# Performance work log

Measured on AMD Instinct MI355X. Metric: run time of the kernel, lower is better.

Reference implementation:

```python
import jax, jax.numpy as jnp
import numpy as np

N = 50000          # nodes
E = 1600000        # edges
H = 8              # heads
F = 16             # out feats per head (np1class)
IN = 256           # in feats
NEG_SLOPE = 0.2    # DGL GATConv default leaky_relu slope


def setup_inputs() -> dict:
    key = jax.random.key(0)
    ks = jax.random.split(key, 7)
    x = jax.random.normal(ks[0], (N, IN), dtype=jnp.float32)
    W = jax.random.normal(ks[1], (IN, H * F), dtype=jnp.float32) * 0.05
    attn_l = jax.random.normal(ks[2], (H, F), dtype=jnp.float32) * 0.05
    attn_r = jax.random.normal(ks[3], (H, F), dtype=jnp.float32) * 0.05
    bias = jax.random.normal(ks[4], (H * F,), dtype=jnp.float32) * 0.05
    src = jax.random.randint(ks[5], (E,), 0, N, dtype=jnp.int64)
    dst = jax.random.randint(ks[6], (E,), 0, N, dtype=jnp.int64)
    return {"x": x, "W": W, "attn_l": attn_l, "attn_r": attn_r,
            "bias": bias, "src": src, "dst": dst}


def reference(x, W, attn_l, attn_r, bias, src, dst):
    # Linear projection to heads: [N, H, F]
    feat = (x @ W).reshape(N, H, F)
    # Per-node attention halves: [N, H]
    el = jnp.einsum('nhf,hf->nh', feat, attn_l)
    er = jnp.einsum('nhf,hf->nh', feat, attn_r)
    # Edge scores: e = leaky_relu(el[src] + er[dst])  -> [E, H]
    e = jax.nn.leaky_relu(el[src] + er[dst], negative_slope=NEG_SLOPE)
    # Segment softmax over incoming edges of each destination node
    m = jax.ops.segment_max(e, dst, num_segments=N)           # [N, H]
    m = jnp.where(jnp.isfinite(m), m, 0.0)                    # empty segments
    m = jax.lax.stop_gradient(m)
    ex = jnp.exp(e - m[dst])                                  # [E, H]
    s = jax.ops.segment_sum(ex, dst, num_segments=N)          # [N, H]
    a = ex / jnp.maximum(s[dst], 1e-9)                        # [E, H]
    # Weighted aggregation of source features: [N, H, F]
    msg = a[:, :, None] * feat[src]
    rst = jax.ops.segment_sum(msg, dst, num_segments=N)
    rst = rst + bias.reshape(H, F)
    # Classifier: mean over heads -> [N, F]
    return rst.mean(axis=1)
```

## Files before the change

### kernel.cpp

```cpp
#include <hip/hip_runtime.h>
#include <hip/hip_bf16.h>

#define NH 8
#define NF 16
#define NIN 256
#define HF 128
#define CAP 3072
#define BCH 4096

typedef __attribute__((ext_vector_type(8))) short bf16x8;
typedef __attribute__((ext_vector_type(4))) float f32x4;

__device__ __forceinline__ unsigned short f2bf(float f) {
    union { float f; unsigned int u; } v; v.f = f;
    unsigned int r = v.u + 0x7FFFu + ((v.u >> 16) & 1u);
    return (unsigned short)(r >> 16);
}
__device__ __forceinline__ float bf2f(unsigned short b) {
    union { unsigned int u; float f; } v; v.u = ((unsigned int)b) << 16;
    return v.f;
}

struct GemmLds {
    union {
        struct {
            unsigned short AsH[32][264];
            unsigned short AsL[32][264];
        };
        float scratch[32][132];
    };
};
struct CsrLds {
    unsigned int eary[CAP];
    unsigned short sSrc[CAP];
    unsigned short roff[512];
    unsigned short rcntl[512];
    int rbase[512];
    int len[64], cur[64];
    unsigned int wsum[4];
    unsigned int sbase;
};
#define POOLSZ ((sizeof(GemmLds) > sizeof(CsrLds)) ? sizeof(GemmLds) : sizeof(CsrLds))

#define GROWS 128
__device__ __forceinline__ void gemm_body(char* pool, int bid,
                                          const float* __restrict__ A,
                                          const float* __restrict__ W,
                                          const float* __restrict__ attn_l,
                                          const float* __restrict__ attn_r,
                                          unsigned short* __restrict__ featb,
                                          float* __restrict__ el,
                                          float* __restrict__ er, int M) {
    GemmLds& gl = *reinterpret_cast<GemmLds*>(pool);
    const int tid = threadIdx.x;
    const int wave = tid >> 6, lane = tid & 63;
    const int quad = lane >> 4, lq = lane & 15;
    const int row0 = bid * GROWS;

    bf16x8 bfrag[8][2];
#pragma unroll
    for (int h2 = 0; h2 < 2; h2++) {
        const int col = (wave * 2 + h2) * 16 + lq;
#pragma unroll
        for (int kk = 0; kk < 8; kk++) {
            const int kb = kk * 32 + quad * 8;
            bf16x8 f;
#pragma unroll
            for (int j = 0; j < 8; j++)
                f[j] = (short)f2bf(W[(size_t)(kb + j) * HF + col]);
            bfrag[kk][h2] = f;
        }
    }

    const int srow = tid >> 3;
    const int erow = tid >> 3, eh = tid & 7;

    for (int c = 0; c < 4; c++) {
        const int crow0 = row0 + c * 32;
        __syncthreads();
#pragma unroll
        for (int i = 0; i < 8; i++) {
            const int col = ((tid & 7) + i * 8) * 4;
            const int gr = crow0 + srow;
            float4 v = make_float4(0.f, 0.f, 0.f, 0.f);
            if (gr < M) v = *(const float4*)&A[(size_t)gr * NIN + col];
            const unsigned short h0 = f2bf(v.x), h1 = f2bf(v.y),
                                 h2b = f2bf(v.z), h3 = f2bf(v.w);
            *(ushort4*)&gl.AsH[srow][col] = make_ushort4(h0, h1, h2b, h3);
            *(ushort4*)&gl.AsL[srow][col] =
                make_ushort4(f2bf(v.x - bf2f(h0)), f2bf(v.y - bf2f(h1)),
                             f2bf(v.z - bf2f(h2b)), f2bf(v.w - bf2f(h3)));
        }
        __syncthreads();
        f32x4 accs[2][2];
#pragma unroll
        for (int s = 0; s < 2; s++) {
            f32x4 acc0 = {0.f, 0.f, 0.f, 0.f};
            f32x4 acc1 = {0.f, 0.f, 0.f, 0.f};
            const int ar = s * 16 + lq;
#pragma unroll
            for (int kk = 0; kk < 8; kk++) {
                const bf16x8 ah = *(const bf16x8*)&gl.AsH[ar][kk * 32 + quad * 8];
                const bf16x8 al = *(const bf16x8*)&gl.AsL[ar][kk * 32 + quad * 8];
                acc0 = __builtin_amdgcn_mfma_f32_16x16x32_bf16(ah, bfrag[kk][0], acc0, 0, 0, 0);
                acc1 = __builtin_amdgcn_mfma_f32_16x16x32_bf16(ah, bfrag[kk][1], acc1, 0, 0, 0);
                acc0 = __builtin_amdgcn_mfma_f32_16x16x32_bf16(al, bfrag[kk][0], acc0, 0, 0, 0);
                acc1 = __builtin_amdgcn_mfma_f32_16x16x32_bf16(al, bfrag[kk][1], acc1, 0, 0, 0);
            }
            accs[s][0] = acc0;
            accs[s][1] = acc1;
#pragma unroll
            for (int r = 0; r < 4; r++) {
                const int gr = crow0 + s * 16 + quad * 4 + r;
                if (gr < M) {
                    featb[(size_t)gr * HF + (wave * 2 + 0) * 16 + lq] = f2bf(acc0[r]);
                    featb[(size_t)gr * HF + (wave * 2 + 1) * 16 + lq] = f2bf(acc1[r]);
                }
            }
        }
        __syncthreads();
#pragma unroll
        for (int s = 0; s < 2; s++)
#pragma unroll
            for (int r = 0; r < 4; r++) {
                const int srw = s * 16 + quad * 4 + r;
                gl.scratch[srw][(wave * 2 + 0) * 16 + lq] = accs[s][0][r];
                gl.scratch[srw][(wave * 2 + 1) * 16 + lq] = accs[s][1][r];
            }
        __syncthreads();
        {
            const int gr = crow0 + erow;
            if (gr < M) {
                const float* sr = &gl.scratch[erow][eh * 16];
                float sl = 0.f, srr = 0.f;
#pragma unroll
                for (int f = 0; f < 16; f++) {
                    const float v = sr[f];
                    sl = fmaf(v, attn_l[eh * 16 + f], sl);
                    srr = fmaf(v, attn_r[eh * 16 + f], srr);
                }
                el[(size_t)gr * NH + eh] = sl;
                er[(size_t)gr * NH + eh] = srr;
            }
        }
    }
}

__device__ __forceinline__ void csr_body(char* pool, int b,
                                         const unsigned int* __restrict__ binned,
                                         const unsigned int* __restrict__ runtab,
                                         int* __restrict__ nodeinfo,
                                         unsigned short* __restrict__ srcsw,
                                         int N, int NB, int nbb) {
    CsrLds& cl = *reinterpret_cast<CsrLds*>(pool);
    const int t = threadIdx.x;
    const int node0 = b << 6;
    const int lane = t & 63, w = t >> 6;
    if (t == 0) cl.sbase = 0;
    __syncthreads();
    for (int c0 = 0; c0 < nbb; c0 += 256) {
        const int r = c0 + t;
        const unsigned int e = (r < nbb) ? runtab[(size_t)r * NB + b] : 0;
        const unsigned int v = e >> 16;
        unsigned int incl = v;
#pragma unroll
        for (int off = 1; off < 64; off <<= 1) {
            const unsigned int x = __shfl_up(incl, off, 64);
            if (lane >= off) incl += x;
        }
        if (lane == 63) cl.wsum[w] = incl;
        __syncthreads();
        unsigned int wbase = 0;
        for (int k = 0; k < w; k++) wbase += cl.wsum[k];
        const unsigned int tot = cl.wsum[0] + cl.wsum[1] + cl.wsum[2] + cl.wsum[3];
        if (r < nbb) {
            cl.roff[r] = (unsigned short)(e & 0xFFFFu);
            cl.rcntl[r] = (unsigned short)v;
            cl.rbase[r] = (int)(cl.sbase + wbase + incl - v);
        }
        __syncthreads();
        if (t == 0) cl.sbase += tot;
        __syncthreads();
    }
    const int tot = (int)cl.sbase;
    for (int r = t; r < nbb; r += 256) {
        const int off = (int)cl.roff[r];
        const int pb = cl.rbase[r];
        const int rc = (int)cl.rcntl[r];
        const unsigned int* bp = &binned[(size_t)r * BCH + off];
        for (int j = 0; j < rc; j++) cl.eary[pb + j] = bp[j];
    }
    if (t < 64) cl.len[t] = 0;
    __syncthreads();
    for (int i = t; i < tot; i += 256) atomicAdd(&cl.len[cl.eary[i] >> 16], 1);
    __syncthreads();
    if (t < 64) {
        const int v = cl.len[t];
        int incl = v;
#pragma unroll
        for (int off = 1; off < 64; off <<= 1) {
            const int x = __shfl_up(incl, off, 64);
            if (t >= off) incl += x;
        }
        const int excl = incl - v;
        cl.cur[t] = excl;
        if (node0 + t < N) nodeinfo[node0 + t] = excl | (v << 16);
    }
    __syncthreads();
    for (int i = t; i < tot; i += 256) {
        const unsigned int p = cl.eary[i];
        const int pos = atomicAdd(&cl.cur[p >> 16], 1);
        cl.sSrc[pos] = (unsigned short)(p & 0xFFFFu);
    }
    __syncthreads();
    unsigned short* sw = &srcsw[(size_t)b * CAP];
    for (int i = t; i < tot; i += 256) sw[i] = cl.sSrc[i];
}

__global__ __launch_bounds__(256) void gemm_csr(const float* __restrict__ A,
                                                const float* __restrict__ W,
                                                const float* __restrict__ attn_l,
                                                const float* __restrict__ attn_r,
                                                unsigned short* __restrict__ featb,
                                                float* __restrict__ el,
                                                float* __restrict__ er, int M,
                                                const unsigned int* __restrict__ binned,
                                                const unsigned int* __restrict__ runtab,
                                                int* __restrict__ nodeinfo,
                                                unsigned short* __restrict__ srcsw,
                                                int NB, int nbb, int GB) {
    __shared__ __align__(16) char pool[POOLSZ];
    if ((int)blockIdx.x < GB)
        gemm_body(pool, blockIdx.x, A, W, attn_l, attn_r, featb, el, er, M);
    else
        csr_body(pool, blockIdx.x - GB, binned, runtab, nodeinfo, srcsw, M, NB, nbb);
}

__global__ __launch_bounds__(256) void bin_kernel(const int* __restrict__ src,
                                                  const int* __restrict__ dst,
                                                  unsigned int* __restrict__ binned,
                                                  unsigned int* __restrict__ runtab,
                                                  int E, int NB) {
    __shared__ unsigned int hist[784];
    __shared__ unsigned int offs[784];
    __shared__ unsigned short lpos[BCH];
    __shared__ unsigned int obuf[BCH];
    __shared__ int dcache[BCH];
    __shared__ unsigned int wsum[4];
    __shared__ unsigned int sbase;
    const int blk = blockIdx.x, t = threadIdx.x;
    const int base = blk * BCH;
    const int cnt = min(BCH, E - base);
    const int lane = t & 63, w = t >> 6;
    for (int b = t; b < NB; b += 256) hist[b] = 0;
    for (int i = t; i < cnt; i += 256) dcache[i] = dst[base + i];
    if (t == 0) sbase = 0;
    __syncthreads();
    for (int i = t; i < cnt; i += 256)
        lpos[i] = (unsigned short)atomicAdd(&hist[dcache[i] >> 6], 1u);
    __syncthreads();
    for (int c0 = 0; c0 < NB; c0 += 256) {
        const int idx = c0 + t;
        const unsigned int v = (idx < NB) ? hist[idx] : 0;
        unsigned int incl = v;
#pragma unroll
        for (int off = 1; off < 64; off <<= 1) {
            const unsigned int x = __shfl_up(incl, off, 64);
            if (lane >= off) incl += x;
        }
        if (lane == 63) wsum[w] = incl;
        __syncthreads();
        unsigned int wbase = 0;
        for (int k = 0; k < w; k++) wbase += wsum[k];
        const unsigned int tot = wsum[0] + wsum[1] + wsum[2] + wsum[3];
        const unsigned int excl = sbase + wbase + incl - v;
        if (idx < NB) {
            offs[idx] = excl;
            runtab[(size_t)blk * NB + idx] = excl | (v << 16);
        }
        __syncthreads();
        if (t == 0) sbase += tot;
        __syncthreads();
    }
    for (int i = t; i < cnt; i += 256) {
        const int d = dcache[i];
        obuf[offs[d >> 6] + lpos[i]] =
            (unsigned int)src[base + i] | ((unsigned int)(d & 63) << 16);
    }
    __syncthreads();
    for (int i = t; i < cnt; i += 256) binned[(size_t)base + i] = obuf[i];
}

#define WIN 64
__global__ __launch_bounds__(256) void agg_kernel(const int* __restrict__ nodeinfo,
                                                  const unsigned short* __restrict__ srcsw,
                                                  const float* __restrict__ el,
                                                  const float* __restrict__ er,
                                                  const unsigned short* __restrict__ featb,
                                                  const float* __restrict__ bias,
                                                  float* __restrict__ out, int N) {
    __shared__ float lds_sc[4][WIN][8];
    __shared__ int lds_src[4][WIN];
    const int tid = threadIdx.x;
    const int w = tid >> 6, lane = tid & 63;
    const int n = blockIdx.x * 4 + w;
    if (n >= N) return;

    const int info = nodeinfo[n];
    const int begin = (n >> 6) * CAP + (info & 0xFFFF);
    const int end = begin + (info >> 16);
    const int hA = lane & 7, eA = lane >> 3;
    const float er_h = er[(size_t)n * NH + hA];
    const int hB = lane >> 3, fB2 = lane & 7;

    float2 acc = make_float2(0.f, 0.f);
    float psum = 0.f;
    for (int base = begin; base < end; base += WIN) {
        const int cn = min(WIN, end - base);
        __builtin_amdgcn_wave_barrier();
#pragma unroll
        for (int rep = 0; rep < 8; rep++) {
            const int ei = rep * 8 + eA;
            if (ei < cn) {
                const int si = (int)srcsw[base + ei];
                if (hA == 0) lds_src[w][ei] = si;
                float v = el[(size_t)si * NH + hA] + er_h;
                v = v > 0.f ? v : 0.2f * v;
                const float sc = __expf(v);
                lds_sc[w][ei][hA] = sc;
                psum += sc;
            }
        }
        __builtin_amdgcn_wave_barrier();
        for (int b0 = 0; b0 < cn; b0 += 16) {
            unsigned int fv[16];
#pragma unroll
            for (int j = 0; j < 16; j++) {
                const int ej = b0 + j;
                const int sj = lds_src[w][ej];
                fv[j] = (ej < cn)
                            ? *(const unsigned int*)&featb[(size_t)sj * HF + hB * 16 + fB2 * 2]
                            : 0u;
            }
#pragma unroll
            for (int j = 0; j < 16; j++) {
                const int ej = b0 + j;
                const float sc = (ej < cn) ? lds_sc[w][ej][hB] : 0.f;
                acc.x = fmaf(sc, bf2f((unsigned short)(fv[j] & 0xFFFFu)), acc.x);
                acc.y = fmaf(sc, bf2f((unsigned short)(fv[j] >> 16)), acc.y);
            }
        }
    }

    float s = psum;
    s += __shfl_xor(s, 8, 64);
    s += __shfl_xor(s, 16, 64);
    s += __shfl_xor(s, 32, 64);
    const float s_h = __shfl(s, hB, 64);
    const float inv = 1.f / fmaxf(s_h, 1e-9f);
    float2 val;
    val.x = acc.x * inv + bias[hB * 16 + fB2 * 2];
    val.y = acc.y * inv + bias[hB * 16 + fB2 * 2 + 1];
    val.x += __shfl_xor(val.x, 8, 64);
    val.x += __shfl_xor(val.x, 16, 64);
    val.x += __shfl_xor(val.x, 32, 64);
    val.y += __shfl_xor(val.y, 8, 64);
    val.y += __shfl_xor(val.y, 16, 64);
    val.y += __shfl_xor(val.y, 32, 64);
    if (lane < 8) {
        float2 o;
        o.x = val.x * 0.125f;
        o.y = val.y * 0.125f;
        *(float2*)&out[(size_t)n * 16 + lane * 2] = o;
    }
}

extern "C" void kernel_launch(void* const* d_in, const int* in_sizes, int n_in,
                              void* d_out, int out_size, void* d_ws, size_t ws_size,
                              hipStream_t stream) {
    const float* x      = (const float*)d_in[0];
    const float* W      = (const float*)d_in[1];
    const float* attn_l = (const float*)d_in[2];
    const float* attn_r = (const float*)d_in[3];
    const float* bias   = (const float*)d_in[4];
    const int*   src    = (const int*)d_in[5];
    const int*   dst    = (const int*)d_in[6];
    float* out = (float*)d_out;

    const int N = in_sizes[0] / NIN;
    const int E = in_sizes[5];
    const int NB = (N + 63) >> 6;
    const int nbb = (E + BCH - 1) / BCH;
    const int GB = (N + GROWS - 1) / GROWS;

    char* w = (char*)d_ws;
    unsigned short* featb = (unsigned short*)w; w += (size_t)N * HF * 2;
    float* el     = (float*)w; w += (size_t)N * NH * 4;
    float* er     = (float*)w; w += (size_t)N * NH * 4;
    int* nodeinfo = (int*)w;   w += (size_t)N * 4;
    unsigned int* binned = (unsigned int*)w; w += (size_t)nbb * BCH * 4;
    unsigned int* runtab = (unsigned int*)w; w += (size_t)nbb * NB * 4;
    unsigned short* srcsw = (unsigned short*)w;

    bin_kernel<<<nbb, 256, 0, stream>>>(src, dst, binned, runtab, E, NB);
    gemm_csr<<<GB + NB, 256, 0, stream>>>(x, W, attn_l, attn_r, featb, el, er, N,
                                          binned, runtab, nodeinfo, srcsw, NB, nbb, GB);
    agg_kernel<<<(N + 3) / 4, 256, 0, stream>>>(nodeinfo, srcsw, el, er, featb, bias,
                                                out, N);
}
```

Before: 209.5 us.

## Fuse edge binning into GEMM/CSR kernel with atomic grid barrier

Moves the edge-binning pass into the combined GEMM/CSR kernel. Binning blocks run alongside the GEMM blocks, wait on a global atomic counter until all binning is finished, then each builds two CSR buckets. This removes a separate kernel launch and the serial dependency between binning and the GEMM. It also narrows the cached dst values to 16 bits to shrink LDS. The spin barrier needs every binning block to be resident at once, so it could deadlock on smaller devices, and it adds a memset to reset the counter.

```diff
diff --git a/kernel.cpp b/kernel.cpp
--- a/kernel.cpp
+++ b/kernel.cpp
@@ -29,6 +29,15 @@
         };
         float scratch[32][132];
     };
+};
+struct BinLds {
+    unsigned short dcache[BCH];
+    unsigned short lpos[BCH];
+    unsigned int hist[784];
+    unsigned int offs[784];
+    unsigned int obuf[BCH];
+    unsigned int wsum[4];
+    unsigned int sbase;
 };
 struct CsrLds {
     unsigned int eary[CAP];
@@ -40,7 +49,8 @@
     unsigned int wsum[4];
     unsigned int sbase;
 };
-#define POOLSZ ((sizeof(GemmLds) > sizeof(CsrLds)) ? sizeof(GemmLds) : sizeof(CsrLds))
+#define MAX2(a,b) ((a) > (b) ? (a) : (b))
+#define POOLSZ MAX2(sizeof(BinLds), MAX2(sizeof(GemmLds), sizeof(CsrLds)))
 
 #define GROWS 128
 __device__ __forceinline__ void gemm_body(char* pool, int bid,
@@ -146,6 +156,56 @@
     }
 }
 
+__device__ __forceinline__ void bin_body(char* pool, int blk,
+                                         const int* __restrict__ src,
+                                         const int* __restrict__ dst,
+                                         unsigned int* __restrict__ binned,
+                                         unsigned int* __restrict__ runtab,
+                                         int E, int NB) {
+    BinLds& bl = *reinterpret_cast<BinLds*>(pool);
+    const int t = threadIdx.x;
+    const int base = blk * BCH;
+    const int cnt = min(BCH, E - base);
+    const int lane = t & 63, w = t >> 6;
+    for (int b = t; b < NB; b += 256) bl.hist[b] = 0;
+    for (int i = t; i < cnt; i += 256) bl.dcache[i] = (unsigned short)dst[base + i];
+    if (t == 0) bl.sbase = 0;
+    __syncthreads();
+    for (int i = t; i < cnt; i += 256)
+        bl.lpos[i] = (unsigned short)atomicAdd(&bl.hist[bl.dcache[i] >> 6], 1u);
+    __syncthreads();
+    for (int c0 = 0; c0 < NB; c0 += 256) {
+        const int idx = c0 + t;
+        const unsigned int v = (idx < NB) ? bl.hist[idx] : 0;
+        unsigned int incl = v;
+#pragma unroll
+        for (int off = 1; off < 64; off <<= 1) {
+            const unsigned int x = __shfl_up(incl, off, 64);
+            if (lane >= off) incl += x;
+        }
+        if (lane == 63) bl.wsum[w] = incl;
+        __syncthreads();
+        unsigned int wbase = 0;
+        for (int k = 0; k < w; k++) wbase += bl.wsum[k];
+        const unsigned int tot = bl.wsum[0] + bl.wsum[1] + bl.wsum[2] + bl.wsum[3];
+        const unsigned int excl = bl.sbase + wbase + incl - v;
+        if (idx < NB) {
+            bl.offs[idx] = excl;
+            runtab[(size_t)blk * NB + idx] = excl | (v << 16);
+        }
+        __syncthreads();
+        if (t == 0) bl.sbase += tot;
+        __syncthreads();
+    }
+    for (int i = t; i < cnt; i += 256) {
+        const int d = (int)bl.dcache[i];
+        bl.obuf[bl.offs[d >> 6] + bl.lpos[i]] =
+            (unsigned int)src[base + i] | ((unsigned int)(d & 63) << 16);
+    }
+    __syncthreads();
+    for (int i = t; i < cnt; i += 256) binned[(size_t)base + i] = bl.obuf[i];
+}
+
 __device__ __forceinline__ void csr_body(char* pool, int b,
                                          const unsigned int* __restrict__ binned,
                                          const unsigned int* __restrict__ runtab,
@@ -217,78 +277,37 @@
     for (int i = t; i < tot; i += 256) sw[i] = cl.sSrc[i];
 }
 
-__global__ __launch_bounds__(256) void gemm_csr(const float* __restrict__ A,
-                                                const float* __restrict__ W,
-                                                const float* __restrict__ attn_l,
-                                                const float* __restrict__ attn_r,
-                                                unsigned short* __restrict__ featb,
-                                                float* __restrict__ el,
-                                                float* __restrict__ er, int M,
-                                                const unsigned int* __restrict__ binned,
-                                                const unsigned int* __restrict__ runtab,
-                                                int* __restrict__ nodeinfo,
-                                                unsigned short* __restrict__ srcsw,
-                                                int NB, int nbb, int GB) {
+__global__ __launch_bounds__(256, 4) void gemm_bincsr(
+        const float* __restrict__ A, const float* __restrict__ W,
+        const float* __restrict__ attn_l, const float* __restrict__ attn_r,
+        unsigned short* __restrict__ featb, float* __restrict__ el,
+        float* __restrict__ er, int M,
+        const int* __restrict__ src, const int* __restrict__ dst,
+        unsigned int* __restrict__ binned, unsigned int* __restrict__ runtab,
+        int* __restrict__ nodeinfo, unsigned short* __restrict__ srcsw,
+        unsigned int* __restrict__ done, int E, int NB, int nbb, int GB) {
     __shared__ __align__(16) char pool[POOLSZ];
-    if ((int)blockIdx.x < GB)
-        gemm_body(pool, blockIdx.x, A, W, attn_l, attn_r, featb, el, er, M);
-    else
-        csr_body(pool, blockIdx.x - GB, binned, runtab, nodeinfo, srcsw, M, NB, nbb);
-}
-
-__global__ __launch_bounds__(256) void bin_kernel(const int* __restrict__ src,
-                                                  const int* __restrict__ dst,
-                                                  unsigned int* __restrict__ binned,
-                                                  unsigned int* __restrict__ runtab,
-                                                  int E, int NB) {
-    __shared__ unsigned int hist[784];
-    __shared__ unsigned int offs[784];
-    __shared__ unsigned short lpos[BCH];
-    __shared__ unsigned int obuf[BCH];
-    __shared__ int dcache[BCH];
-    __shared__ unsigned int wsum[4];
-    __shared__ unsigned int sbase;
-    const int blk = blockIdx.x, t = threadIdx.x;
-    const int base = blk * BCH;
-    const int cnt = min(BCH, E - base);
-    const int lane = t & 63, w = t >> 6;
-    for (int b = t; b < NB; b += 256) hist[b] = 0;
-    for (int i = t; i < cnt; i += 256) dcache[i] = dst[base + i];
-    if (t == 0) sbase = 0;
-    __syncthreads();
-    for (int i = t; i < cnt; i += 256)
-        lpos[i] = (unsigned short)atomicAdd(&hist[dcache[i] >> 6], 1u);
-    __syncthreads();
-    for (int c0 = 0; c0 < NB; c0 += 256) {
-        const int idx = c0 + t;
-        const unsigned int v = (idx < NB) ? hist[idx] : 0;
-        unsigned int incl = v;
-#pragma unroll
-        for (int off = 1; off < 64; off <<= 1) {
-            const unsigned int x = __shfl_up(incl, off, 64);
-            if (lane >= off) incl += x;
-        }
-        if (lane == 63) wsum[w] = incl;
-        __syncthreads();
-        unsigned int wbase = 0;
-        for (int k = 0; k < w; k++) wbase += wsum[k];
-        const unsigned int tot = wsum[0] + wsum[1] + wsum[2] + wsum[3];
-        const unsigned int excl = sbase + wbase + incl - v;
-        if (idx < NB) {
-            offs[idx] = excl;
-            runtab[(size_t)blk * NB + idx] = excl | (v << 16);
-        }
-        __syncthreads();
-        if (t == 0) sbase += tot;
-        __syncthreads();
-    }
-    for (int i = t; i < cnt; i += 256) {
-        const int d = dcache[i];
-        obuf[offs[d >> 6] + lpos[i]] =
-            (unsigned int)src[base + i] | ((unsigned int)(d & 63) << 16);
-    }
-    __syncthreads();
-    for (int i = t; i < cnt; i += 256) binned[(size_t)base + i] = obuf[i];
+    const int bid = (int)blockIdx.x;
+    if (bid < GB) {
+        gemm_body(pool, bid, A, W, attn_l, attn_r, featb, el, er, M);
+        return;
+    }
+    const int bb = bid - GB;
+    bin_body(pool, bb, src, dst, binned, runtab, E, NB);
+    __syncthreads();
+    if (threadIdx.x == 0) {
+        __threadfence();
+        atomicAdd(done, 1u);
+        while (__hip_atomic_load(done, __ATOMIC_RELAXED, __HIP_MEMORY_SCOPE_AGENT)
+               < (unsigned)nbb)
+            __builtin_amdgcn_s_sleep(8);
+    }
+    __syncthreads();
+    __threadfence();
+    csr_body(pool, 2 * bb, binned, runtab, nodeinfo, srcsw, M, NB, nbb);
+    __syncthreads();
+    if (2 * bb + 1 < NB)
+        csr_body(pool, 2 * bb + 1, binned, runtab, nodeinfo, srcsw, M, NB, nbb);
 }
 
 #define WIN 64
@@ -400,11 +419,13 @@
     int* nodeinfo = (int*)w;   w += (size_t)N * 4;
     unsigned int* binned = (unsigned int*)w; w += (size_t)nbb * BCH * 4;
     unsigned int* runtab = (unsigned int*)w; w += (size_t)nbb * NB * 4;
-    unsigned short* srcsw = (unsigned short*)w;
-
-    bin_kernel<<<nbb, 256, 0, stream>>>(src, dst, binned, runtab, E, NB);
-    gemm_csr<<<GB + NB, 256, 0, stream>>>(x, W, attn_l, attn_r, featb, el, er, N,
-                                          binned, runtab, nodeinfo, srcsw, NB, nbb, GB);
+    unsigned short* srcsw = (unsigned short*)w; w += (size_t)NB * CAP * 2;
+    unsigned int* done = (unsigned int*)w;
+
+    hipMemsetAsync(done, 0, 4, stream);
+    gemm_bincsr<<<GB + nbb, 256, 0, stream>>>(x, W, attn_l, attn_r, featb, el, er, N,
+                                              src, dst, binned, runtab, nodeinfo,
+                                              srcsw, done, E, NB, nbb, GB);
     agg_kernel<<<(N + 3) / 4, 256, 0, stream>>>(nodeinfo, srcsw, el, er, featb, bias,
                                                 out, N);
 }
```

New measurement: 285.5 us. +36.3%, slower.
